# Kernel optimization log

Measured on AMD Instinct MI355X. Metric: run time of the kernel, lower is better.

## Reference

```python
import jax, jax.numpy as jnp
import numpy as np

HEAD_NUM = 8
EMB = 256
HEAD_SIZE = EMB // HEAD_NUM
POS_LEN = 128
ROPE_BASE = 100.0
LN_EPS = 1e-5
SOFTPICK_EPS = 1e-6


def _rope_tables():
    inv_freq = 1.0 / ROPE_BASE ** (jnp.arange(0, HEAD_SIZE, 2, dtype=jnp.float32) / HEAD_SIZE)
    t = jnp.arange(POS_LEN, dtype=jnp.float32)
    freqs = jnp.einsum('i,j->ij', t, inv_freq)          # [W, hs/2]
    freqs = jnp.concatenate([freqs, freqs], axis=-1)     # [W, hs]
    return jnp.sin(freqs), jnp.cos(freqs)


def _apply_rope(e, sin, cos):
    # e: [..., W, hs]; sin/cos: [W, hs]
    h = HEAD_SIZE // 2
    rot = jnp.concatenate([-e[..., h:], e[..., :h]], axis=-1)
    return e * cos + rot * sin


def _layernorm(x, g, b):
    mu = jnp.mean(x, axis=-1, keepdims=True)
    var = jnp.mean(jnp.square(x - mu), axis=-1, keepdims=True)
    return (x - mu) * jax.lax.rsqrt(var + LN_EPS) * g + b


def _softpick(x):
    m = jnp.max(x, axis=-1, keepdims=True)
    e = jnp.exp(x - m) - jnp.exp(-m)
    return jax.nn.relu(e) / (jnp.sum(jnp.abs(e), axis=-1, keepdims=True) + SOFTPICK_EPS)


def setup_inputs() -> dict:
    key = jax.random.key(0)
    ks = jax.random.split(key, 12)
    B, C, H, W = 4, EMB, 256, 128
    hn, hs = HEAD_NUM, HEAD_SIZE
    s = 0.02
    return {
        'left': jax.random.normal(ks[0], (B, C, H, W), jnp.float32),
        'right': jax.random.normal(ks[1], (B, C, H, W), jnp.float32),
        'qw': jax.random.normal(ks[2], (hn, hs, hs), jnp.float32) * s,   # grouped 1x1 conv weights
        'kw': jax.random.normal(ks[3], (hn, hs, hs), jnp.float32) * s,
        'vw': jax.random.normal(ks[4], (hn, hs, hs), jnp.float32) * s,
        'proj_w': jax.random.normal(ks[5], (C, C), jnp.float32) * s,
        'proj_b': jnp.zeros((C,), jnp.float32),
        'ln1_g': jnp.ones((C,), jnp.float32),
        'ln1_b': jnp.zeros((C,), jnp.float32),
        'ln2_g': jnp.ones((C,), jnp.float32),
        'ln2_b': jnp.zeros((C,), jnp.float32),
        'w1': jax.random.normal(ks[6], (C, 4 * C), jnp.float32) * s,
        'b1': jnp.zeros((4 * C,), jnp.float32),
        'w2': jax.random.normal(ks[7], (4 * C, C), jnp.float32) * s,
        'b2': jnp.zeros((C,), jnp.float32),
    }


def reference(left, right, qw, kw, vw, proj_w, proj_b,
              ln1_g, ln1_b, ln2_g, ln2_b, w1, b1, w2, b2):
    B, C, H, W = left.shape
    hn, hs = HEAD_NUM, HEAD_SIZE
    scale = hs ** -0.5
    sin, cos = _rope_tables()  # [W, hs]

    def grouped_proj(x, w):
        # grouped 1x1 conv -> per-head matmul; out [B, H, hn, W, hs]
        xr = x.reshape(B, hn, hs, H, W)
        return jnp.einsum('bgihw,goi->bhgwo', xr, w)

    q = _apply_rope(grouped_proj(left, qw), sin, cos)
    k = _apply_rope(grouped_proj(right, kw), sin, cos)
    v = grouped_proj(right, vw)

    att = _softpick(jnp.einsum('bhgqd,bhgkd->bhgqk', q, k) * scale)  # [B,H,hn,W,W]
    out = jnp.einsum('bhgqk,bhgkd->bhqgd', att, v).reshape(B, H, W, C)

    x1 = _layernorm(out @ proj_w + proj_b + jnp.transpose(left, (0, 2, 3, 1)), ln1_g, ln1_b)
    ffn = jax.nn.gelu(x1 @ w1 + b1, approximate=False) @ w2 + b2
    return _layernorm(ffn + x1, ln2_g, ln2_b)
```

## Files before the change

kernel.cpp:

```cpp
#include <hip/hip_runtime.h>
#include <hip/hip_bf16.h>

#define DEV __device__ __forceinline__

typedef __attribute__((ext_vector_type(8))) short bf16x8_t;
typedef __attribute__((ext_vector_type(4))) float f32x4_t;

constexpr int cB = 4, cC = 256, cH = 256, cW = 128, cHN = 8, cHS = 32;
constexpr int cM = cB * cH * cW;

DEV float bfu(unsigned int b16) { union { unsigned int u; float f; } v; v.u = b16 << 16; return v.f; }
DEV unsigned short f2bb(float f) { union { __hip_bfloat16 h; unsigned short u; } v; v.h = __float2bfloat16(f); return v.u; }
DEV unsigned int pk2(float a, float b) { return (unsigned)f2bb(a) | ((unsigned)f2bb(b) << 16); }

#define GLOAD_LDS16(g, l) \
  __builtin_amdgcn_global_load_lds((const __attribute__((address_space(1))) void*)(g), \
                                   (__attribute__((address_space(3))) void*)(l), 16, 0, 0)

DEV float gelu_fast(float v) {
  float ax = fabsf(v) * 0.7071067811865475f;
  float t = __builtin_amdgcn_rcpf(1.0f + 0.3275911f * ax);
  float poly = ((((1.061405429f * t - 1.453152027f) * t + 1.421413741f) * t
                 - 0.284496736f) * t + 0.254829592f) * t;
  float e = __expf(-ax * ax);
  float erfv = 1.0f - poly * e;
  float phi = 0.5f + 0.5f * copysignf(erfv, v);
  return v * phi;
}

__global__ __launch_bounds__(256) void transpose_bf16(const float* __restrict__ src,
                                                      __hip_bfloat16* __restrict__ dst,
                                                      int R, int Ccol) {
  int idx = blockIdx.x * 256 + threadIdx.x;
  if (idx < R * Ccol) {
    int r = idx / Ccol, c = idx - r * Ccol;
    dst[c * R + r] = __float2bfloat16(src[idx]);
  }
}

__global__ __launch_bounds__(256) void transpose_perm_bf16(const float* __restrict__ src,
                                                           __hip_bfloat16* __restrict__ dst,
                                                           int R, int Ccol) {
  int idx = blockIdx.x * 256 + threadIdx.x;
  if (idx < R * Ccol) {
    int r = idx / Ccol, c = idx - r * Ccol;
    int pk = (r & ~63) | ((r & 15) << 2) | ((r >> 4) & 3);
    dst[c * R + pk] = __float2bfloat16(src[idx]);
  }
}

__global__ __launch_bounds__(256) void rope_init(float2* __restrict__ tab) {
  int i = blockIdx.x * 256 + threadIdx.x;
  int w = i >> 4, c = i & 15;
  float inv = expf((float)c * -0.28782313662425572f);
  float ang = (float)w * inv;
  tab[i] = make_float2(sinf(ang), cosf(ang));
}

constexpr int XL_OFF = 0, XR_OFF = 10240, WQ_OFF = 20480, WK_OFF = 23040, WV_OFF = 25600;
constexpr int QS_OFF = 28160, KS_OFF = 38400, VT_OFF = 0, P_OFF = 10240;
constexpr int SMEM_BYTES = 48640;

__global__ __launch_bounds__(256) void attn_mfma(
    const float* __restrict__ left, const float* __restrict__ right,
    const float* __restrict__ qw, const float* __restrict__ kw, const float* __restrict__ vw,
    const float2* __restrict__ rope,
    __hip_bfloat16* __restrict__ att_out)
{
  __shared__ __align__(16) char smem[SMEM_BYTES];

  const int t = threadIdx.x;
  const int g = blockIdx.x & 7;
  const int h = (blockIdx.x >> 3) & 255;
  const int b = blockIdx.x >> 11;
  const size_t HW = (size_t)cH * cW;

  {
    const float* lb = left  + ((size_t)(b * cC + g * cHS) * cH + h) * cW;
    const float* rb = right + ((size_t)(b * cC + g * cHS) * cH + h) * cW;
    int w = t & 127, ih = (t >> 7) * 16;
    unsigned short* xlrow = (unsigned short*)(smem + XL_OFF) + w * 40 + ih;
    unsigned short* xrrow = (unsigned short*)(smem + XR_OFF) + w * 40 + ih;
#pragma unroll
    for (int i = 0; i < 16; i += 2) {
      float a0 = lb[(size_t)(ih + i) * HW + w], a1 = lb[(size_t)(ih + i + 1) * HW + w];
      *(unsigned int*)(xlrow + i) = pk2(a0, a1);
      float c0 = rb[(size_t)(ih + i) * HW + w], c1 = rb[(size_t)(ih + i + 1) * HW + w];
      *(unsigned int*)(xrrow + i) = pk2(c0, c1);
    }
    int o = t >> 3, i0 = (t & 7) * 4;
    {
      float4 v4 = *(const float4*)(qw + g * 1024 + t * 4);
      unsigned short* dst = (unsigned short*)(smem + WQ_OFF) + o * 40 + i0;
      *(unsigned int*)(dst) = pk2(v4.x, v4.y); *(unsigned int*)(dst + 2) = pk2(v4.z, v4.w);
    }
    {
      float4 v4 = *(const float4*)(kw + g * 1024 + t * 4);
      unsigned short* dst = (unsigned short*)(smem + WK_OFF) + o * 40 + i0;
      *(unsigned int*)(dst) = pk2(v4.x, v4.y); *(unsigned int*)(dst + 2) = pk2(v4.z, v4.w);
    }
    {
      float4 v4 = *(const float4*)(vw + g * 1024 + t * 4);
      unsigned short* dst = (unsigned short*)(smem + WV_OFF) + o * 40 + i0;
      *(unsigned int*)(dst) = pk2(v4.x, v4.y); *(unsigned int*)(dst + 2) = pk2(v4.z, v4.w);
    }
  }
  __syncthreads();

  const int lane = t & 63, wid = t >> 6;
  const int c = lane & 15, q4 = lane >> 4;
  const int wbase = wid * 32;
  const f32x4_t zero = {0.f, 0.f, 0.f, 0.f};

  bf16x8_t a_xl[2], a_xr[2];
#pragma unroll
  for (int sub = 0; sub < 2; ++sub) {
    a_xl[sub] = *(const bf16x8_t*)(smem + XL_OFF + (wbase + sub * 16 + c) * 80 + q4 * 16);
    a_xr[sub] = *(const bf16x8_t*)(smem + XR_OFF + (wbase + sub * 16 + c) * 80 + q4 * 16);
  }
  f32x4_t qacc[2][2], kacc[2][2];
#pragma unroll
  for (int ot = 0; ot < 2; ++ot) {
    bf16x8_t bq = *(const bf16x8_t*)(smem + WQ_OFF + (ot * 16 + c) * 80 + q4 * 16);
    bf16x8_t bk = *(const bf16x8_t*)(smem + WK_OFF + (ot * 16 + c) * 80 + q4 * 16);
#pragma unroll
    for (int sub = 0; sub < 2; ++sub) {
      qacc[sub][ot] = __builtin_amdgcn_mfma_f32_16x16x32_bf16(a_xl[sub], bq, zero, 0, 0, 0);
      kacc[sub][ot] = __builtin_amdgcn_mfma_f32_16x16x32_bf16(a_xr[sub], bk, zero, 0, 0, 0);
    }
  }
  {
    const float scale = 0.17677669529663687f;
    unsigned short* qsp = (unsigned short*)(smem + QS_OFF);
    unsigned short* ksp = (unsigned short*)(smem + KS_OFF);
#pragma unroll
    for (int sub = 0; sub < 2; ++sub)
#pragma unroll
      for (int r = 0; r < 4; ++r) {
        int w = wbase + sub * 16 + q4 * 4 + r;
        float2 sc = rope[w * 16 + c];
        float sn = sc.x, cs = sc.y;
        float q0 = qacc[sub][0][r], q1 = qacc[sub][1][r];
        qsp[w * 40 + c]      = f2bb((q0 * cs - q1 * sn) * scale);
        qsp[w * 40 + c + 16] = f2bb((q1 * cs + q0 * sn) * scale);
        float k0 = kacc[sub][0][r], k1 = kacc[sub][1][r];
        ksp[w * 40 + c]      = f2bb(k0 * cs - k1 * sn);
        ksp[w * 40 + c + 16] = f2bb(k1 * cs + k0 * sn);
      }
  }
  __syncthreads();

  {
    f32x4_t vacc[2][2];
#pragma unroll
    for (int dt = 0; dt < 2; ++dt) {
      bf16x8_t awv = *(const bf16x8_t*)(smem + WV_OFF + (dt * 16 + c) * 80 + q4 * 16);
#pragma unroll
      for (int sub = 0; sub < 2; ++sub)
        vacc[dt][sub] = __builtin_amdgcn_mfma_f32_16x16x32_bf16(awv, a_xr[sub], zero, 0, 0, 0);
    }
    unsigned short* vtp = (unsigned short*)(smem + VT_OFF);
#pragma unroll
    for (int dt = 0; dt < 2; ++dt)
#pragma unroll
      for (int r = 0; r < 4; ++r) {
        int d = dt * 16 + q4 * 4 + r;
        *(unsigned int*)(vtp + d * 136 + c * 8 + wid * 2) = pk2(vacc[dt][0][r], vacc[dt][1][r]);
      }
  }

  bf16x8_t aq0 = *(const bf16x8_t*)(smem + QS_OFF + (wbase + c) * 80 + q4 * 16);
  bf16x8_t aq1 = *(const bf16x8_t*)(smem + QS_OFF + (wbase + 16 + c) * 80 + q4 * 16);
  f32x4_t sac[2][8];
#pragma unroll
  for (int kt = 0; kt < 8; ++kt) {
    bf16x8_t bk = *(const bf16x8_t*)(smem + KS_OFF + (kt * 16 + c) * 80 + q4 * 16);
    sac[0][kt] = __builtin_amdgcn_mfma_f32_16x16x32_bf16(aq0, bk, zero, 0, 0, 0);
    sac[1][kt] = __builtin_amdgcn_mfma_f32_16x16x32_bf16(aq1, bk, zero, 0, 0, 0);
  }

  float dinv_[2][4];
#pragma unroll
  for (int sub = 0; sub < 2; ++sub)
#pragma unroll
    for (int r = 0; r < 4; ++r) {
      float m = sac[sub][0][r];
#pragma unroll
      for (int kt = 1; kt < 8; ++kt) m = fmaxf(m, sac[sub][kt][r]);
      m = fmaxf(m, __shfl_xor(m, 1));
      m = fmaxf(m, __shfl_xor(m, 2));
      m = fmaxf(m, __shfl_xor(m, 4));
      m = fmaxf(m, __shfl_xor(m, 8));
      float em = __expf(-m);
      float ss = 0.f;
#pragma unroll
      for (int kt = 0; kt < 8; ++kt) {
        float e = __expf(sac[sub][kt][r] - m) - em;
        sac[sub][kt][r] = fmaxf(e, 0.f);
        ss += fabsf(e);
      }
      ss += __shfl_xor(ss, 1);
      ss += __shfl_xor(ss, 2);
      ss += __shfl_xor(ss, 4);
      ss += __shfl_xor(ss, 8);
      dinv_[sub][r] = 1.0f / (ss + 1e-6f);
    }
  __syncthreads();

  {
    unsigned short* pp = (unsigned short*)(smem + P_OFF);
#pragma unroll
    for (int sub = 0; sub < 2; ++sub)
#pragma unroll
      for (int r = 0; r < 4; ++r) {
        int w = wbase + sub * 16 + q4 * 4 + r;
        float dv = dinv_[sub][r];
        uint4 u;
        u.x = pk2(sac[sub][0][r] * dv, sac[sub][1][r] * dv);
        u.y = pk2(sac[sub][2][r] * dv, sac[sub][3][r] * dv);
        u.z = pk2(sac[sub][4][r] * dv, sac[sub][5][r] * dv);
        u.w = pk2(sac[sub][6][r] * dv, sac[sub][7][r] * dv);
        *(uint4*)(pp + w * 136 + c * 8) = u;
      }
  }
  f32x4_t oacc[2][2] = {{zero, zero}, {zero, zero}};
#pragma unroll
  for (int ks = 0; ks < 4; ++ks) {
    bf16x8_t ap0 = *(const bf16x8_t*)(smem + P_OFF + (wbase + c) * 272 + ks * 64 + q4 * 16);
    bf16x8_t ap1 = *(const bf16x8_t*)(smem + P_OFF + (wbase + 16 + c) * 272 + ks * 64 + q4 * 16);
    bf16x8_t bv0 = *(const bf16x8_t*)(smem + VT_OFF + (c) * 272 + ks * 64 + q4 * 16);
    bf16x8_t bv1 = *(const bf16x8_t*)(smem + VT_OFF + (16 + c) * 272 + ks * 64 + q4 * 16);
    oacc[0][0] = __builtin_amdgcn_mfma_f32_16x16x32_bf16(ap0, bv0, oacc[0][0], 0, 0, 0);
    oacc[0][1] = __builtin_amdgcn_mfma_f32_16x16x32_bf16(ap0, bv1, oacc[0][1], 0, 0, 0);
    oacc[1][0] = __builtin_amdgcn_mfma_f32_16x16x32_bf16(ap1, bv0, oacc[1][0], 0, 0, 0);
    oacc[1][1] = __builtin_amdgcn_mfma_f32_16x16x32_bf16(ap1, bv1, oacc[1][1], 0, 0, 0);
  }
  {
    __hip_bfloat16* ob = att_out + ((size_t)(b * cH + h) * cW) * cC + g * cHS;
#pragma unroll
    for (int sub = 0; sub < 2; ++sub)
#pragma unroll
      for (int dt = 0; dt < 2; ++dt)
#pragma unroll
        for (int r = 0; r < 4; ++r) {
          int w = wbase + sub * 16 + q4 * 4 + r;
          ob[(size_t)w * cC + dt * 16 + c] = __float2bfloat16(oacc[sub][dt][r]);
        }
  }
}

__global__ __launch_bounds__(256) void ffn1_gemm(
    const __hip_bfloat16* __restrict__ A, const __hip_bfloat16* __restrict__ Bt,
    const float* __restrict__ bias, __hip_bfloat16* __restrict__ outb)
{
  constexpr int K = 256, N = 1024;
  __shared__ __align__(16) char smem[49152];
  const int t = threadIdx.x;
  const int id = blockIdx.x;
  const int slot = id >> 3;
  const int by = (id & 7) * 128 + (slot >> 3);
  const int bx = slot & 7;
  const int m0 = by * 128, n0 = bx * 128;
  const int lane = t & 63, wid = t >> 6;
  const int r16 = lane & 15, kq = lane >> 4;
  const int wr = (wid >> 1) * 64, wc = (wid & 1) * 64;

  f32x4_t acc[4][4];
#pragma unroll
  for (int fi = 0; fi < 4; ++fi)
#pragma unroll
    for (int fj = 0; fj < 4; ++fj) acc[fi][fj] = {0.f, 0.f, 0.f, 0.f};

  auto stage = [&](int buf, int k0) {
    char* As = smem + buf * 16384;
    char* Bs = As + 8192;
#pragma unroll
    for (int i = 0; i < 2; ++i) {
      int chunk = i * 4 + wid;
      int row = chunk * 16 + (lane >> 2);
      int sw = (((lane & 3) ^ ((row >> 1) & 3))) * 8;
      GLOAD_LDS16(A  + (size_t)(m0 + row) * K + k0 + sw, As + chunk * 1024);
      GLOAD_LDS16(Bt + (size_t)(n0 + row) * K + k0 + sw, Bs + chunk * 1024);
    }
  };

  constexpr int NK = K >> 5;
  stage(0, 0);
  stage(1, 32);
  for (int tt = 0; tt < NK; ++tt) {
    if (tt + 2 < NK) {
      stage((tt + 2) % 3, (tt + 2) << 5);
      asm volatile("s_waitcnt vmcnt(8)" ::: "memory");
    } else if (tt + 1 < NK) {
      asm volatile("s_waitcnt vmcnt(4)" ::: "memory");
    } else {
      asm volatile("s_waitcnt vmcnt(0)" ::: "memory");
    }
    __builtin_amdgcn_s_barrier();
    __builtin_amdgcn_sched_barrier(0);
    char* As = smem + (tt % 3) * 16384;
    char* Bs = As + 8192;
    bf16x8_t af[4], bf[4];
#pragma unroll
    for (int fi = 0; fi < 4; ++fi) {
      int rr = wr + fi * 16 + r16;
      af[fi] = *(const bf16x8_t*)(As + rr * 64 + ((kq ^ ((rr >> 1) & 3)) * 16));
    }
#pragma unroll
    for (int fj = 0; fj < 4; ++fj) {
      int rr = wc + fj * 16 + r16;
      bf[fj] = *(const bf16x8_t*)(Bs + rr * 64 + ((kq ^ ((rr >> 1) & 3)) * 16));
    }
#pragma unroll
    for (int fi = 0; fi < 4; ++fi)
#pragma unroll
      for (int fj = 0; fj < 4; ++fj)
        acc[fi][fj] = __builtin_amdgcn_mfma_f32_16x16x32_bf16(af[fi], bf[fj], acc[fi][fj], 0, 0, 0);
    __builtin_amdgcn_sched_barrier(0);
    __builtin_amdgcn_s_barrier();
  }

  float bv[4];
#pragma unroll
  for (int fj = 0; fj < 4; ++fj) bv[fj] = bias[n0 + wc + fj * 16 + r16];
  __hip_bfloat16* obase = outb + (size_t)(m0 + wr + kq * 4) * N + n0 + wc + r16 * 4;
#pragma unroll
  for (int fi = 0; fi < 4; ++fi)
#pragma unroll
    for (int r = 0; r < 4; ++r) {
      float v0 = gelu_fast(acc[fi][0][r] + bv[0]);
      float v1 = gelu_fast(acc[fi][1][r] + bv[1]);
      float v2 = gelu_fast(acc[fi][2][r] + bv[2]);
      float v3 = gelu_fast(acc[fi][3][r] + bv[3]);
      uint2 u;
      u.x = pk2(v0, v1);
      u.y = pk2(v2, v3);
      *(uint2*)(obase + (size_t)(fi * 16 + r) * N) = u;
    }
}

template<int KK, bool FFN2>
__global__ __launch_bounds__(256, 2) void gemm_ln(
    const __hip_bfloat16* __restrict__ A, const __hip_bfloat16* __restrict__ Bt,
    const float* __restrict__ bias, const float* __restrict__ leftres,
    const __hip_bfloat16* __restrict__ resbf,
    const float* __restrict__ g, const float* __restrict__ be,
    void* __restrict__ outp)
{
  __shared__ __align__(16) char smem[73728];
  const int t = threadIdx.x, lane = t & 63, wid = t >> 6;
  const int c = lane & 15, q4 = lane >> 4;
  const int m0 = blockIdx.x * 128;
  const int wr = wid * 32;
  const f32x4_t zero = {0.f, 0.f, 0.f, 0.f};

  f32x4_t acc[2][16];
#pragma unroll
  for (int fi = 0; fi < 2; ++fi)
#pragma unroll
    for (int fj = 0; fj < 16; ++fj) acc[fi][fj] = zero;

  auto stage = [&](int buf, int k0) {
    char* As = smem + buf * 24576;
    char* Bs = As + 8192;
#pragma unroll
    for (int i = 0; i < 2; ++i) {
      int chunk = (wid * 2 + i);
      int row = chunk * 16 + (lane >> 2);
      int sw = (((lane & 3) ^ ((row >> 1) & 3))) * 8;
      GLOAD_LDS16(A + (size_t)(m0 + row) * KK + k0 + sw, As + chunk * 1024);
    }
#pragma unroll
    for (int i = 0; i < 4; ++i) {
      int chunk = (wid * 4 + i);
      int row = chunk * 16 + (lane >> 2);
      int sw = (((lane & 3) ^ ((row >> 1) & 3))) * 8;
      GLOAD_LDS16(Bt + (size_t)row * KK + k0 + sw, Bs + chunk * 1024);
    }
  };

  constexpr int NK = KK >> 5;
  stage(0, 0);
  stage(1, 32);
  for (int tt = 0; tt < NK; ++tt) {
    if (tt + 2 < NK) {
      stage((tt + 2) % 3, (tt + 2) << 5);
      asm volatile("s_waitcnt vmcnt(12)" ::: "memory");
    } else if (tt + 1 < NK) {
      asm volatile("s_waitcnt vmcnt(6)" ::: "memory");
    } else {
      asm volatile("s_waitcnt vmcnt(0)" ::: "memory");
    }
    __builtin_amdgcn_s_barrier();
    __builtin_amdgcn_sched_barrier(0);
    char* As = smem + (tt % 3) * 24576;
    char* Bs = As + 8192;
    int ra0 = wr + c, ra1 = wr + 16 + c;
    bf16x8_t af0 = *(const bf16x8_t*)(As + ra0 * 64 + ((q4 ^ ((ra0 >> 1) & 3)) * 16));
    bf16x8_t af1 = *(const bf16x8_t*)(As + ra1 * 64 + ((q4 ^ ((ra1 >> 1) & 3)) * 16));
#pragma unroll
    for (int fj = 0; fj < 16; ++fj) {
      int rb = fj * 16 + c;
      bf16x8_t bf = *(const bf16x8_t*)(Bs + rb * 64 + ((q4 ^ ((rb >> 1) & 3)) * 16));
      acc[0][fj] = __builtin_amdgcn_mfma_f32_16x16x32_bf16(af0, bf, acc[0][fj], 0, 0, 0);
      acc[1][fj] = __builtin_amdgcn_mfma_f32_16x16x32_bf16(af1, bf, acc[1][fj], 0, 0, 0);
    }
    __builtin_amdgcn_sched_barrier(0);
    __builtin_amdgcn_s_barrier();
  }

  if (!FFN2) {
    const int b_ = m0 >> 15, h_ = (m0 >> 7) & 255;
#pragma unroll
    for (int fj = 0; fj < 16; ++fj) {
      int n = fj * 16 + c;
      float bv = bias[n];
#pragma unroll
      for (int fi = 0; fi < 2; ++fi) {
        int w0 = wr + fi * 16 + q4 * 4;
        float4 lr = *(const float4*)(leftres + (((size_t)b_ * 256 + n) * 256 + h_) * 128 + w0);
        float la[4] = {lr.x, lr.y, lr.z, lr.w};
#pragma unroll
        for (int r = 0; r < 4; ++r) acc[fi][fj][r] += bv + la[r];
      }
    }
  } else {
#pragma unroll
    for (int fj = 0; fj < 16; ++fj) {
      int n = fj * 16 + c;
      float bv = bias[n];
#pragma unroll
      for (int fi = 0; fi < 2; ++fi)
#pragma unroll
        for (int r = 0; r < 4; ++r) {
          int row = wr + fi * 16 + q4 * 4 + r;
          acc[fi][fj][r] += bv + __bfloat162float(resbf[(size_t)(m0 + row) * 256 + n]);
        }
    }
  }

  float mu[2][4], rs[2][4];
#pragma unroll
  for (int fi = 0; fi < 2; ++fi)
#pragma unroll
    for (int r = 0; r < 4; ++r) {
      float s = 0.f;
#pragma unroll
      for (int fj = 0; fj < 16; ++fj) s += acc[fi][fj][r];
      s += __shfl_xor(s, 1); s += __shfl_xor(s, 2); s += __shfl_xor(s, 4); s += __shfl_xor(s, 8);
      float m_ = s * (1.0f / 256.0f);
      float sq = 0.f;
#pragma unroll
      for (int fj = 0; fj < 16; ++fj) { float d = acc[fi][fj][r] - m_; sq += d * d; }
      sq += __shfl_xor(sq, 1); sq += __shfl_xor(sq, 2); sq += __shfl_xor(sq, 4); sq += __shfl_xor(sq, 8);
      mu[fi][r] = m_;
      rs[fi][r] = rsqrtf(sq * (1.0f / 256.0f) + 1e-5f);
    }
#pragma unroll
  for (int fj = 0; fj < 16; ++fj) {
    int n = fj * 16 + c;
    float gv = g[n], bev = be[n];
#pragma unroll
    for (int fi = 0; fi < 2; ++fi)
#pragma unroll
      for (int r = 0; r < 4; ++r) {
        int row = wr + fi * 16 + q4 * 4 + r;
        float val = (acc[fi][fj][r] - mu[fi][r]) * rs[fi][r] * gv + bev;
        if (FFN2)
          ((float*)outp)[(size_t)(m0 + row) * 256 + n] = val;
        else
          ((__hip_bfloat16*)outp)[(size_t)(m0 + row) * 256 + n] = __float2bfloat16(val);
      }
  }
}

extern "C" void kernel_launch(void* const* d_in, const int* in_sizes, int n_in,
                              void* d_out, int out_size, void* d_ws, size_t ws_size,
                              hipStream_t stream) {
  const float* left   = (const float*)d_in[0];
  const float* right  = (const float*)d_in[1];
  const float* qw     = (const float*)d_in[2];
  const float* kw     = (const float*)d_in[3];
  const float* vw     = (const float*)d_in[4];
  const float* proj_w = (const float*)d_in[5];
  const float* proj_b = (const float*)d_in[6];
  const float* ln1_g  = (const float*)d_in[7];
  const float* ln1_b  = (const float*)d_in[8];
  const float* ln2_g  = (const float*)d_in[9];
  const float* ln2_b  = (const float*)d_in[10];
  const float* w1     = (const float*)d_in[11];
  const float* b1     = (const float*)d_in[12];
  const float* w2     = (const float*)d_in[13];
  const float* b2     = (const float*)d_in[14];

  char* ws = (char*)d_ws;
  __hip_bfloat16* att_out = (__hip_bfloat16*)ws;
  __hip_bfloat16* x1      = (__hip_bfloat16*)(ws + 67108864);
  __hip_bfloat16* hidden  = (__hip_bfloat16*)(ws + 134217728);
  float2*         rope    = (float2*)(ws + 134217728);
  __hip_bfloat16* pwT     = (__hip_bfloat16*)(ws + 402653184);
  __hip_bfloat16* w1T     = pwT + 65536;
  __hip_bfloat16* w2T     = w1T + 262144;

  transpose_bf16<<<256, 256, 0, stream>>>(proj_w, pwT, 256, 256);
  transpose_bf16<<<1024, 256, 0, stream>>>(w1, w1T, 256, 1024);
  transpose_perm_bf16<<<1024, 256, 0, stream>>>(w2, w2T, 1024, 256);
  rope_init<<<8, 256, 0, stream>>>(rope);

  attn_mfma<<<cB * cH * cHN, 256, 0, stream>>>(left, right, qw, kw, vw, rope, att_out);

  gemm_ln<256, false><<<cM / 128, 256, 0, stream>>>(att_out, pwT, proj_b, left, nullptr,
                                                    ln1_g, ln1_b, x1);
  ffn1_gemm<<<8192, 256, 0, stream>>>(x1, w1T, b1, hidden);
  gemm_ln<1024, true><<<cM / 128, 256, 0, stream>>>(hidden, w2T, b2, nullptr, x1,
                                                    ln2_g, ln2_b, d_out);
}
```

Measured before the change: 445.1 us.

## Store FFN hidden and W2 in scaled FP8 and use FP8 MFMA for FFN2

The GELU output of FFN1 is now scaled by 64 and packed to FP8 instead of bf16, and W2 is transposed into scaled FP8. A new FFN2+LayerNorm kernel runs fp8×fp8 MFMA and unscales by 1/4096 before the residual and norm. This halves the dominant hidden-tensor traffic (written by FFN1, read by FFN2) and uses a higher-throughput MFMA path. The cost is lower precision, which risks accuracy against the reference tolerance.

```diff
diff --git a/kernel.cpp b/kernel.cpp
--- a/kernel.cpp
+++ b/kernel.cpp
@@ -38,14 +38,15 @@
   }
 }
 
-__global__ __launch_bounds__(256) void transpose_perm_bf16(const float* __restrict__ src,
-                                                           __hip_bfloat16* __restrict__ dst,
-                                                           int R, int Ccol) {
+__global__ __launch_bounds__(256) void transpose_perm_fp8(const float* __restrict__ src,
+                                                          unsigned char* __restrict__ dst,
+                                                          int R, int Ccol) {
   int idx = blockIdx.x * 256 + threadIdx.x;
   if (idx < R * Ccol) {
     int r = idx / Ccol, c = idx - r * Ccol;
     int pk = (r & ~63) | ((r & 15) << 2) | ((r >> 4) & 3);
-    dst[c * R + pk] = __float2bfloat16(src[idx]);
+    int u = __builtin_amdgcn_cvt_pk_fp8_f32(src[idx] * 64.0f, 0.0f, 0, false);
+    dst[(size_t)c * R + pk] = (unsigned char)(u & 0xff);
   }
 }
 
@@ -251,7 +252,7 @@
 
 __global__ __launch_bounds__(256) void ffn1_gemm(
     const __hip_bfloat16* __restrict__ A, const __hip_bfloat16* __restrict__ Bt,
-    const float* __restrict__ bias, __hip_bfloat16* __restrict__ outb)
+    const float* __restrict__ bias, unsigned char* __restrict__ outb)
 {
   constexpr int K = 256, N = 1024;
   __shared__ __align__(16) char smem[49152];
@@ -323,30 +324,28 @@
   float bv[4];
 #pragma unroll
   for (int fj = 0; fj < 4; ++fj) bv[fj] = bias[n0 + wc + fj * 16 + r16];
-  __hip_bfloat16* obase = outb + (size_t)(m0 + wr + kq * 4) * N + n0 + wc + r16 * 4;
+  unsigned char* obase = outb + (size_t)(m0 + wr + kq * 4) * N + n0 + wc + r16 * 4;
 #pragma unroll
   for (int fi = 0; fi < 4; ++fi)
 #pragma unroll
     for (int r = 0; r < 4; ++r) {
-      float v0 = gelu_fast(acc[fi][0][r] + bv[0]);
-      float v1 = gelu_fast(acc[fi][1][r] + bv[1]);
-      float v2 = gelu_fast(acc[fi][2][r] + bv[2]);
-      float v3 = gelu_fast(acc[fi][3][r] + bv[3]);
-      uint2 u;
-      u.x = pk2(v0, v1);
-      u.y = pk2(v2, v3);
-      *(uint2*)(obase + (size_t)(fi * 16 + r) * N) = u;
-    }
-}
-
-template<int KK, bool FFN2>
-__global__ __launch_bounds__(256, 2) void gemm_ln(
+      float v0 = gelu_fast(acc[fi][0][r] + bv[0]) * 64.0f;
+      float v1 = gelu_fast(acc[fi][1][r] + bv[1]) * 64.0f;
+      float v2 = gelu_fast(acc[fi][2][r] + bv[2]) * 64.0f;
+      float v3 = gelu_fast(acc[fi][3][r] + bv[3]) * 64.0f;
+      int u = __builtin_amdgcn_cvt_pk_fp8_f32(v0, v1, 0, false);
+      u = __builtin_amdgcn_cvt_pk_fp8_f32(v2, v3, u, true);
+      *(unsigned int*)(obase + (size_t)(fi * 16 + r) * N) = (unsigned)u;
+    }
+}
+
+__global__ __launch_bounds__(256, 2) void proj_gemm_ln(
     const __hip_bfloat16* __restrict__ A, const __hip_bfloat16* __restrict__ Bt,
     const float* __restrict__ bias, const float* __restrict__ leftres,
-    const __hip_bfloat16* __restrict__ resbf,
     const float* __restrict__ g, const float* __restrict__ be,
-    void* __restrict__ outp)
+    __hip_bfloat16* __restrict__ outp)
 {
+  constexpr int KK = 256;
   __shared__ __align__(16) char smem[73728];
   const int t = threadIdx.x, lane = t & 63, wid = t >> 6;
   const int c = lane & 15, q4 = lane >> 4;
@@ -409,7 +408,7 @@
     __builtin_amdgcn_s_barrier();
   }
 
-  if (!FFN2) {
+  {
     const int b_ = m0 >> 15, h_ = (m0 >> 7) & 255;
 #pragma unroll
     for (int fj = 0; fj < 16; ++fj) {
@@ -424,19 +423,6 @@
         for (int r = 0; r < 4; ++r) acc[fi][fj][r] += bv + la[r];
       }
     }
-  } else {
-#pragma unroll
-    for (int fj = 0; fj < 16; ++fj) {
-      int n = fj * 16 + c;
-      float bv = bias[n];
-#pragma unroll
-      for (int fi = 0; fi < 2; ++fi)
-#pragma unroll
-        for (int r = 0; r < 4; ++r) {
-          int row = wr + fi * 16 + q4 * 4 + r;
-          acc[fi][fj][r] += bv + __bfloat162float(resbf[(size_t)(m0 + row) * 256 + n]);
-        }
-    }
   }
 
   float mu[2][4], rs[2][4];
@@ -465,11 +451,132 @@
 #pragma unroll
       for (int r = 0; r < 4; ++r) {
         int row = wr + fi * 16 + q4 * 4 + r;
-        float val = (acc[fi][fj][r] - mu[fi][r]) * rs[fi][r] * gv + bev;
-        if (FFN2)
-          ((float*)outp)[(size_t)(m0 + row) * 256 + n] = val;
-        else
-          ((__hip_bfloat16*)outp)[(size_t)(m0 + row) * 256 + n] = __float2bfloat16(val);
+        outp[(size_t)(m0 + row) * 256 + n] =
+            __float2bfloat16((acc[fi][fj][r] - mu[fi][r]) * rs[fi][r] * gv + bev);
+      }
+  }
+}
+
+__global__ __launch_bounds__(256, 2) void ffn2_ln(
+    const unsigned char* __restrict__ A, const unsigned char* __restrict__ Bt,
+    const float* __restrict__ bias, const __hip_bfloat16* __restrict__ resbf,
+    const float* __restrict__ g, const float* __restrict__ be,
+    float* __restrict__ outp)
+{
+  constexpr int KK = 1024;
+  __shared__ __align__(16) char smem[73728];
+  const int t = threadIdx.x, lane = t & 63, wid = t >> 6;
+  const int c = lane & 15, q4 = lane >> 4;
+  const int m0 = blockIdx.x * 128;
+  const int wr = wid * 32;
+  const f32x4_t zero = {0.f, 0.f, 0.f, 0.f};
+
+  f32x4_t acc[2][16];
+#pragma unroll
+  for (int fi = 0; fi < 2; ++fi)
+#pragma unroll
+    for (int fj = 0; fj < 16; ++fj) acc[fi][fj] = zero;
+
+  auto stage = [&](int buf, int k0) {
+    char* As = smem + buf * 24576;
+    char* Bs = As + 8192;
+#pragma unroll
+    for (int i = 0; i < 2; ++i) {
+      int chunk = (wid * 2 + i);
+      int row = chunk * 16 + (lane >> 2);
+      int sw = (((lane & 3) ^ ((row >> 1) & 3))) * 16;
+      GLOAD_LDS16(A + (size_t)(m0 + row) * KK + k0 + sw, As + chunk * 1024);
+    }
+#pragma unroll
+    for (int i = 0; i < 4; ++i) {
+      int chunk = (wid * 4 + i);
+      int row = chunk * 16 + (lane >> 2);
+      int sw = (((lane & 3) ^ ((row >> 1) & 3))) * 16;
+      GLOAD_LDS16(Bt + (size_t)row * KK + k0 + sw, Bs + chunk * 1024);
+    }
+  };
+
+  constexpr int NK = 16;
+  stage(0, 0);
+  stage(1, 64);
+  const int sl = (c >> 1) & 3;
+  const int koff0 = ((((q4 >> 1)) ^ sl) << 4) | ((q4 & 1) << 3);
+  const int koff1 = (((2 | (q4 >> 1)) ^ sl) << 4) | ((q4 & 1) << 3);
+  for (int tt = 0; tt < NK; ++tt) {
+    if (tt + 2 < NK) {
+      stage((tt + 2) % 3, (tt + 2) << 6);
+      asm volatile("s_waitcnt vmcnt(12)" ::: "memory");
+    } else if (tt + 1 < NK) {
+      asm volatile("s_waitcnt vmcnt(6)" ::: "memory");
+    } else {
+      asm volatile("s_waitcnt vmcnt(0)" ::: "memory");
+    }
+    __builtin_amdgcn_s_barrier();
+    __builtin_amdgcn_sched_barrier(0);
+    char* As = smem + (tt % 3) * 24576;
+    char* Bs = As + 8192;
+    const char* arow0 = As + (wr + c) * 64;
+    const char* arow1 = As + (wr + 16 + c) * 64;
+    long a00 = *(const long*)(arow0 + koff0);
+    long a01 = *(const long*)(arow0 + koff1);
+    long a10 = *(const long*)(arow1 + koff0);
+    long a11 = *(const long*)(arow1 + koff1);
+#pragma unroll
+    for (int fj = 0; fj < 16; ++fj) {
+      const char* brow = Bs + (fj * 16 + c) * 64;
+      long b0 = *(const long*)(brow + koff0);
+      long b1 = *(const long*)(brow + koff1);
+      acc[0][fj] = __builtin_amdgcn_mfma_f32_16x16x32_fp8_fp8(a00, b0, acc[0][fj], 0, 0, 0);
+      acc[0][fj] = __builtin_amdgcn_mfma_f32_16x16x32_fp8_fp8(a01, b1, acc[0][fj], 0, 0, 0);
+      acc[1][fj] = __builtin_amdgcn_mfma_f32_16x16x32_fp8_fp8(a10, b0, acc[1][fj], 0, 0, 0);
+      acc[1][fj] = __builtin_amdgcn_mfma_f32_16x16x32_fp8_fp8(a11, b1, acc[1][fj], 0, 0, 0);
+    }
+    __builtin_amdgcn_sched_barrier(0);
+    __builtin_amdgcn_s_barrier();
+  }
+
+#pragma unroll
+  for (int fj = 0; fj < 16; ++fj) {
+    int n = fj * 16 + c;
+    float bv = bias[n];
+#pragma unroll
+    for (int fi = 0; fi < 2; ++fi)
+#pragma unroll
+      for (int r = 0; r < 4; ++r) {
+        int row = wr + fi * 16 + q4 * 4 + r;
+        acc[fi][fj][r] = acc[fi][fj][r] * 0.000244140625f + bv +
+                         __bfloat162float(resbf[(size_t)(m0 + row) * 256 + n]);
+      }
+  }
+
+  float mu[2][4], rs[2][4];
+#pragma unroll
+  for (int fi = 0; fi < 2; ++fi)
+#pragma unroll
+    for (int r = 0; r < 4; ++r) {
+      float s = 0.f;
+#pragma unroll
+      for (int fj = 0; fj < 16; ++fj) s += acc[fi][fj][r];
+      s += __shfl_xor(s, 1); s += __shfl_xor(s, 2); s += __shfl_xor(s, 4); s += __shfl_xor(s, 8);
+      float m_ = s * (1.0f / 256.0f);
+      float sq = 0.f;
+#pragma unroll
+      for (int fj = 0; fj < 16; ++fj) { float d = acc[fi][fj][r] - m_; sq += d * d; }
+      sq += __shfl_xor(sq, 1); sq += __shfl_xor(sq, 2); sq += __shfl_xor(sq, 4); sq += __shfl_xor(sq, 8);
+      mu[fi][r] = m_;
+      rs[fi][r] = rsqrtf(sq * (1.0f / 256.0f) + 1e-5f);
+    }
+#pragma unroll
+  for (int fj = 0; fj < 16; ++fj) {
+    int n = fj * 16 + c;
+    float gv = g[n], bev = be[n];
+#pragma unroll
+    for (int fi = 0; fi < 2; ++fi)
+#pragma unroll
+      for (int r = 0; r < 4; ++r) {
+        int row = wr + fi * 16 + q4 * 4 + r;
+        outp[(size_t)(m0 + row) * 256 + n] =
+            (acc[fi][fj][r] - mu[fi][r]) * rs[fi][r] * gv + bev;
       }
   }
 }
@@ -496,22 +603,20 @@
   char* ws = (char*)d_ws;
   __hip_bfloat16* att_out = (__hip_bfloat16*)ws;
   __hip_bfloat16* x1      = (__hip_bfloat16*)(ws + 67108864);
-  __hip_bfloat16* hidden  = (__hip_bfloat16*)(ws + 134217728);
+  unsigned char*  hidden  = (unsigned char*)(ws + 134217728);
   float2*         rope    = (float2*)(ws + 134217728);
   __hip_bfloat16* pwT     = (__hip_bfloat16*)(ws + 402653184);
   __hip_bfloat16* w1T     = pwT + 65536;
-  __hip_bfloat16* w2T     = w1T + 262144;
+  unsigned char*  w2T     = (unsigned char*)(w1T + 262144);
 
   transpose_bf16<<<256, 256, 0, stream>>>(proj_w, pwT, 256, 256);
   transpose_bf16<<<1024, 256, 0, stream>>>(w1, w1T, 256, 1024);
-  transpose_perm_bf16<<<1024, 256, 0, stream>>>(w2, w2T, 1024, 256);
+  transpose_perm_fp8<<<1024, 256, 0, stream>>>(w2, w2T, 1024, 256);
   rope_init<<<8, 256, 0, stream>>>(rope);
 
   attn_mfma<<<cB * cH * cHN, 256, 0, stream>>>(left, right, qw, kw, vw, rope, att_out);
 
-  gemm_ln<256, false><<<cM / 128, 256, 0, stream>>>(att_out, pwT, proj_b, left, nullptr,
-                                                    ln1_g, ln1_b, x1);
+  proj_gemm_ln<<<cM / 128, 256, 0, stream>>>(att_out, pwT, proj_b, left, ln1_g, ln1_b, x1);
   ffn1_gemm<<<8192, 256, 0, stream>>>(x1, w1T, b1, hidden);
-  gemm_ln<1024, true><<<cM / 128, 256, 0, stream>>>(hidden, w2T, b2, nullptr, x1,
-                                                    ln2_g, ln2_b, d_out);
-}
+  ffn2_ln<<<cM / 128, 256, 0, stream>>>(hidden, w2T, b2, x1, ln2_g, ln2_b, (float*)d_out);
+}
```

Measured after the change: 406.4 us, median of 2. -8.7%, faster.

## Fuse FFN1 GEMM+GELU with FFN2 GEMM+LayerNorm into one kernel

Applied to the files above, without the earlier changes.

The separate FFN1 GEMM (which wrote a 1024-wide bf16 hidden tensor to global memory) and the FFN2 GEMM+LN kernel are replaced by a single kernel. Each block keeps a 128-row x1 tile in LDS and loops over 32-column hidden chunks, computing GELU(x1·W1) into LDS and accumulating it straight into the 256-wide output accumulators. The residual is read from the LDS copy of x1, and the w2 permutation changes to suit the 32-wide k-chunks. This removes the large hidden-tensor round trip through HBM, but uses about 136KB of LDS, so only one block fits per CU, and adds barriers inside every chunk iteration.

```diff
diff --git a/kernel.cpp b/kernel.cpp
--- a/kernel.cpp
+++ b/kernel.cpp
@@ -38,14 +38,14 @@
   }
 }
 
-__global__ __launch_bounds__(256) void transpose_perm_bf16(const float* __restrict__ src,
-                                                           __hip_bfloat16* __restrict__ dst,
-                                                           int R, int Ccol) {
+__global__ __launch_bounds__(256) void transpose_perm32_bf16(const float* __restrict__ src,
+                                                             __hip_bfloat16* __restrict__ dst,
+                                                             int R, int Ccol) {
   int idx = blockIdx.x * 256 + threadIdx.x;
   if (idx < R * Ccol) {
     int r = idx / Ccol, c = idx - r * Ccol;
-    int pk = (r & ~63) | ((r & 15) << 2) | ((r >> 4) & 3);
-    dst[c * R + pk] = __float2bfloat16(src[idx]);
+    int pk = (r & ~31) | ((r & 15) << 1) | ((r >> 4) & 1);
+    dst[(size_t)c * R + pk] = __float2bfloat16(src[idx]);
   }
 }
 
@@ -249,104 +249,13 @@
   }
 }
 
-__global__ __launch_bounds__(256) void ffn1_gemm(
-    const __hip_bfloat16* __restrict__ A, const __hip_bfloat16* __restrict__ Bt,
-    const float* __restrict__ bias, __hip_bfloat16* __restrict__ outb)
-{
-  constexpr int K = 256, N = 1024;
-  __shared__ __align__(16) char smem[49152];
-  const int t = threadIdx.x;
-  const int id = blockIdx.x;
-  const int slot = id >> 3;
-  const int by = (id & 7) * 128 + (slot >> 3);
-  const int bx = slot & 7;
-  const int m0 = by * 128, n0 = bx * 128;
-  const int lane = t & 63, wid = t >> 6;
-  const int r16 = lane & 15, kq = lane >> 4;
-  const int wr = (wid >> 1) * 64, wc = (wid & 1) * 64;
-
-  f32x4_t acc[4][4];
-#pragma unroll
-  for (int fi = 0; fi < 4; ++fi)
-#pragma unroll
-    for (int fj = 0; fj < 4; ++fj) acc[fi][fj] = {0.f, 0.f, 0.f, 0.f};
-
-  auto stage = [&](int buf, int k0) {
-    char* As = smem + buf * 16384;
-    char* Bs = As + 8192;
-#pragma unroll
-    for (int i = 0; i < 2; ++i) {
-      int chunk = i * 4 + wid;
-      int row = chunk * 16 + (lane >> 2);
-      int sw = (((lane & 3) ^ ((row >> 1) & 3))) * 8;
-      GLOAD_LDS16(A  + (size_t)(m0 + row) * K + k0 + sw, As + chunk * 1024);
-      GLOAD_LDS16(Bt + (size_t)(n0 + row) * K + k0 + sw, Bs + chunk * 1024);
-    }
-  };
-
-  constexpr int NK = K >> 5;
-  stage(0, 0);
-  stage(1, 32);
-  for (int tt = 0; tt < NK; ++tt) {
-    if (tt + 2 < NK) {
-      stage((tt + 2) % 3, (tt + 2) << 5);
-      asm volatile("s_waitcnt vmcnt(8)" ::: "memory");
-    } else if (tt + 1 < NK) {
-      asm volatile("s_waitcnt vmcnt(4)" ::: "memory");
-    } else {
-      asm volatile("s_waitcnt vmcnt(0)" ::: "memory");
-    }
-    __builtin_amdgcn_s_barrier();
-    __builtin_amdgcn_sched_barrier(0);
-    char* As = smem + (tt % 3) * 16384;
-    char* Bs = As + 8192;
-    bf16x8_t af[4], bf[4];
-#pragma unroll
-    for (int fi = 0; fi < 4; ++fi) {
-      int rr = wr + fi * 16 + r16;
-      af[fi] = *(const bf16x8_t*)(As + rr * 64 + ((kq ^ ((rr >> 1) & 3)) * 16));
-    }
-#pragma unroll
-    for (int fj = 0; fj < 4; ++fj) {
-      int rr = wc + fj * 16 + r16;
-      bf[fj] = *(const bf16x8_t*)(Bs + rr * 64 + ((kq ^ ((rr >> 1) & 3)) * 16));
-    }
-#pragma unroll
-    for (int fi = 0; fi < 4; ++fi)
-#pragma unroll
-      for (int fj = 0; fj < 4; ++fj)
-        acc[fi][fj] = __builtin_amdgcn_mfma_f32_16x16x32_bf16(af[fi], bf[fj], acc[fi][fj], 0, 0, 0);
-    __builtin_amdgcn_sched_barrier(0);
-    __builtin_amdgcn_s_barrier();
-  }
-
-  float bv[4];
-#pragma unroll
-  for (int fj = 0; fj < 4; ++fj) bv[fj] = bias[n0 + wc + fj * 16 + r16];
-  __hip_bfloat16* obase = outb + (size_t)(m0 + wr + kq * 4) * N + n0 + wc + r16 * 4;
-#pragma unroll
-  for (int fi = 0; fi < 4; ++fi)
-#pragma unroll
-    for (int r = 0; r < 4; ++r) {
-      float v0 = gelu_fast(acc[fi][0][r] + bv[0]);
-      float v1 = gelu_fast(acc[fi][1][r] + bv[1]);
-      float v2 = gelu_fast(acc[fi][2][r] + bv[2]);
-      float v3 = gelu_fast(acc[fi][3][r] + bv[3]);
-      uint2 u;
-      u.x = pk2(v0, v1);
-      u.y = pk2(v2, v3);
-      *(uint2*)(obase + (size_t)(fi * 16 + r) * N) = u;
-    }
-}
-
-template<int KK, bool FFN2>
-__global__ __launch_bounds__(256, 2) void gemm_ln(
+__global__ __launch_bounds__(256, 2) void proj_gemm_ln(
     const __hip_bfloat16* __restrict__ A, const __hip_bfloat16* __restrict__ Bt,
     const float* __restrict__ bias, const float* __restrict__ leftres,
-    const __hip_bfloat16* __restrict__ resbf,
     const float* __restrict__ g, const float* __restrict__ be,
-    void* __restrict__ outp)
+    __hip_bfloat16* __restrict__ outp)
 {
+  constexpr int KK = 256;
   __shared__ __align__(16) char smem[73728];
   const int t = threadIdx.x, lane = t & 63, wid = t >> 6;
   const int c = lane & 15, q4 = lane >> 4;
@@ -409,7 +318,7 @@
     __builtin_amdgcn_s_barrier();
   }
 
-  if (!FFN2) {
+  {
     const int b_ = m0 >> 15, h_ = (m0 >> 7) & 255;
 #pragma unroll
     for (int fj = 0; fj < 16; ++fj) {
@@ -424,19 +333,6 @@
         for (int r = 0; r < 4; ++r) acc[fi][fj][r] += bv + la[r];
       }
     }
-  } else {
-#pragma unroll
-    for (int fj = 0; fj < 16; ++fj) {
-      int n = fj * 16 + c;
-      float bv = bias[n];
-#pragma unroll
-      for (int fi = 0; fi < 2; ++fi)
-#pragma unroll
-        for (int r = 0; r < 4; ++r) {
-          int row = wr + fi * 16 + q4 * 4 + r;
-          acc[fi][fj][r] += bv + __bfloat162float(resbf[(size_t)(m0 + row) * 256 + n]);
-        }
-    }
   }
 
   float mu[2][4], rs[2][4];
@@ -465,11 +361,164 @@
 #pragma unroll
       for (int r = 0; r < 4; ++r) {
         int row = wr + fi * 16 + q4 * 4 + r;
-        float val = (acc[fi][fj][r] - mu[fi][r]) * rs[fi][r] * gv + bev;
-        if (FFN2)
-          ((float*)outp)[(size_t)(m0 + row) * 256 + n] = val;
-        else
-          ((__hip_bfloat16*)outp)[(size_t)(m0 + row) * 256 + n] = __float2bfloat16(val);
+        outp[(size_t)(m0 + row) * 256 + n] =
+            __float2bfloat16((acc[fi][fj][r] - mu[fi][r]) * rs[fi][r] * gv + bev);
+      }
+  }
+}
+
+__global__ __launch_bounds__(256, 1) void ffn_fused2(
+    const __hip_bfloat16* __restrict__ x1g, const __hip_bfloat16* __restrict__ w1T,
+    const __hip_bfloat16* __restrict__ w2T, const float* __restrict__ b1,
+    const float* __restrict__ b2, const float* __restrict__ g2, const float* __restrict__ be2,
+    float* __restrict__ outp)
+{
+  __shared__ __align__(16) char smem[139264];
+  char* X1  = smem;
+  char* W1b = smem + 65536;
+  char* W2b = smem + 98304;
+  char* H   = smem + 131072;
+
+  const int t = threadIdx.x, lane = t & 63, wid = t >> 6;
+  const int c = lane & 15, q4 = lane >> 4;
+  const int m0 = blockIdx.x * 128;
+  const int wr = wid * 32;
+  const f32x4_t zero = {0.f, 0.f, 0.f, 0.f};
+  const int sw8 = c & 7;
+  const int sw4 = (c >> 1) & 3;
+
+#pragma unroll
+  for (int i = 0; i < 16; ++i) {
+    int L = i * 256 + t;
+    int row = L >> 5, s = lane & 31;
+    int gsl = s ^ (row & 7);
+    GLOAD_LDS16(x1g + (size_t)(m0 + row) * 256 + gsl * 8, X1 + (i * 4096 + wid * 1024));
+  }
+
+  auto stageW = [&](int buf, int j) {
+    char* W1 = W1b + buf * 16384;
+    char* W2 = W2b + buf * 16384;
+#pragma unroll
+    for (int i = 0; i < 4; ++i) {
+      int L = i * 256 + t;
+      int row = L >> 5, s = lane & 31;
+      int gsl = s ^ (row & 7);
+      GLOAD_LDS16(w1T + (size_t)(j * 32 + row) * 256 + gsl * 8, W1 + (i * 4096 + wid * 1024));
+    }
+#pragma unroll
+    for (int i = 0; i < 4; ++i) {
+      int L = i * 256 + t;
+      int row = L >> 2, s = lane & 3;
+      int gsl = s ^ ((row >> 1) & 3);
+      GLOAD_LDS16(w2T + (size_t)row * 1024 + j * 32 + gsl * 8, W2 + (i * 4096 + wid * 1024));
+    }
+  };
+  stageW(0, 0);
+
+  f32x4_t acc[2][16];
+#pragma unroll
+  for (int fi = 0; fi < 2; ++fi)
+#pragma unroll
+    for (int fj = 0; fj < 16; ++fj) acc[fi][fj] = zero;
+
+  for (int j = 0; j < 32; ++j) {
+    if (j + 1 < 32) {
+      stageW((j + 1) & 1, j + 1);
+      asm volatile("s_waitcnt vmcnt(8)" ::: "memory");
+    } else {
+      asm volatile("s_waitcnt vmcnt(0)" ::: "memory");
+    }
+    __builtin_amdgcn_s_barrier();
+    __builtin_amdgcn_sched_barrier(0);
+
+    char* W1 = W1b + (j & 1) * 16384;
+    f32x4_t hacc[2][2] = {{zero, zero}, {zero, zero}};
+#pragma unroll
+    for (int kk = 0; kk < 8; ++kk) {
+      int sl = (kk * 4 + q4) ^ sw8;
+      bf16x8_t a0 = *(const bf16x8_t*)(X1 + (wr + c) * 512 + sl * 16);
+      bf16x8_t a1 = *(const bf16x8_t*)(X1 + (wr + 16 + c) * 512 + sl * 16);
+      bf16x8_t b0 = *(const bf16x8_t*)(W1 + (c) * 512 + sl * 16);
+      bf16x8_t b1f = *(const bf16x8_t*)(W1 + (16 + c) * 512 + sl * 16);
+      hacc[0][0] = __builtin_amdgcn_mfma_f32_16x16x32_bf16(a0, b0, hacc[0][0], 0, 0, 0);
+      hacc[0][1] = __builtin_amdgcn_mfma_f32_16x16x32_bf16(a0, b1f, hacc[0][1], 0, 0, 0);
+      hacc[1][0] = __builtin_amdgcn_mfma_f32_16x16x32_bf16(a1, b0, hacc[1][0], 0, 0, 0);
+      hacc[1][1] = __builtin_amdgcn_mfma_f32_16x16x32_bf16(a1, b1f, hacc[1][1], 0, 0, 0);
+    }
+
+    float b1v0 = b1[j * 32 + c], b1v1 = b1[j * 32 + 16 + c];
+#pragma unroll
+    for (int fi = 0; fi < 2; ++fi)
+#pragma unroll
+      for (int r = 0; r < 4; ++r) {
+        int row = wr + fi * 16 + q4 * 4 + r;
+        float v0 = gelu_fast(hacc[fi][0][r] + b1v0);
+        float v1 = gelu_fast(hacc[fi][1][r] + b1v1);
+        int swv = (q4 * 2 + (r >> 1)) & 3;
+        *(unsigned int*)(H + row * 64 + (((c >> 2) ^ swv) * 16) + (c & 3) * 4) = pk2(v0, v1);
+      }
+    __builtin_amdgcn_sched_barrier(0);
+    asm volatile("s_waitcnt lgkmcnt(0)" ::: "memory");
+    __builtin_amdgcn_s_barrier();
+    __builtin_amdgcn_sched_barrier(0);
+
+    char* W2 = W2b + (j & 1) * 16384;
+    int slh = q4 ^ sw4;
+    bf16x8_t ha0 = *(const bf16x8_t*)(H + (wr + c) * 64 + slh * 16);
+    bf16x8_t ha1 = *(const bf16x8_t*)(H + (wr + 16 + c) * 64 + slh * 16);
+#pragma unroll
+    for (int fj = 0; fj < 16; ++fj) {
+      int rb = fj * 16 + c;
+      bf16x8_t wb = *(const bf16x8_t*)(W2 + rb * 64 + ((q4 ^ ((rb >> 1) & 3)) * 16));
+      acc[0][fj] = __builtin_amdgcn_mfma_f32_16x16x32_bf16(ha0, wb, acc[0][fj], 0, 0, 0);
+      acc[1][fj] = __builtin_amdgcn_mfma_f32_16x16x32_bf16(ha1, wb, acc[1][fj], 0, 0, 0);
+    }
+    __builtin_amdgcn_sched_barrier(0);
+  }
+
+#pragma unroll
+  for (int fj = 0; fj < 16; ++fj) {
+    int n = fj * 16 + c;
+    float bv = b2[n];
+#pragma unroll
+    for (int fi = 0; fi < 2; ++fi)
+#pragma unroll
+      for (int r = 0; r < 4; ++r) {
+        int row = wr + fi * 16 + q4 * 4 + r;
+        int swr = (q4 * 4 + r) & 7;
+        int gsl = (fj * 2 + (c >> 3)) ^ swr;
+        unsigned short rv = *(unsigned short*)(X1 + row * 512 + gsl * 16 + (c & 7) * 2);
+        acc[fi][fj][r] += bv + bfu(rv);
+      }
+  }
+  float mu[2][4], rs[2][4];
+#pragma unroll
+  for (int fi = 0; fi < 2; ++fi)
+#pragma unroll
+    for (int r = 0; r < 4; ++r) {
+      float s = 0.f;
+#pragma unroll
+      for (int fj = 0; fj < 16; ++fj) s += acc[fi][fj][r];
+      s += __shfl_xor(s, 1); s += __shfl_xor(s, 2); s += __shfl_xor(s, 4); s += __shfl_xor(s, 8);
+      float m_ = s * (1.0f / 256.0f);
+      float sq = 0.f;
+#pragma unroll
+      for (int fj = 0; fj < 16; ++fj) { float d = acc[fi][fj][r] - m_; sq += d * d; }
+      sq += __shfl_xor(sq, 1); sq += __shfl_xor(sq, 2); sq += __shfl_xor(sq, 4); sq += __shfl_xor(sq, 8);
+      mu[fi][r] = m_;
+      rs[fi][r] = rsqrtf(sq * (1.0f / 256.0f) + 1e-5f);
+    }
+#pragma unroll
+  for (int fj = 0; fj < 16; ++fj) {
+    int n = fj * 16 + c;
+    float gv = g2[n], bev = be2[n];
+#pragma unroll
+    for (int fi = 0; fi < 2; ++fi)
+#pragma unroll
+      for (int r = 0; r < 4; ++r) {
+        int row = wr + fi * 16 + q4 * 4 + r;
+        outp[(size_t)(m0 + row) * 256 + n] =
+            (acc[fi][fj][r] - mu[fi][r]) * rs[fi][r] * gv + bev;
       }
   }
 }
@@ -496,7 +545,6 @@
   char* ws = (char*)d_ws;
   __hip_bfloat16* att_out = (__hip_bfloat16*)ws;
   __hip_bfloat16* x1      = (__hip_bfloat16*)(ws + 67108864);
-  __hip_bfloat16* hidden  = (__hip_bfloat16*)(ws + 134217728);
   float2*         rope    = (float2*)(ws + 134217728);
   __hip_bfloat16* pwT     = (__hip_bfloat16*)(ws + 402653184);
   __hip_bfloat16* w1T     = pwT + 65536;
@@ -504,14 +552,11 @@
 
   transpose_bf16<<<256, 256, 0, stream>>>(proj_w, pwT, 256, 256);
   transpose_bf16<<<1024, 256, 0, stream>>>(w1, w1T, 256, 1024);
-  transpose_perm_bf16<<<1024, 256, 0, stream>>>(w2, w2T, 1024, 256);
+  transpose_perm32_bf16<<<1024, 256, 0, stream>>>(w2, w2T, 1024, 256);
   rope_init<<<8, 256, 0, stream>>>(rope);
 
   attn_mfma<<<cB * cH * cHN, 256, 0, stream>>>(left, right, qw, kw, vw, rope, att_out);
 
-  gemm_ln<256, false><<<cM / 128, 256, 0, stream>>>(att_out, pwT, proj_b, left, nullptr,
-                                                    ln1_g, ln1_b, x1);
-  ffn1_gemm<<<8192, 256, 0, stream>>>(x1, w1T, b1, hidden);
-  gemm_ln<1024, true><<<cM / 128, 256, 0, stream>>>(hidden, w2T, b2, nullptr, x1,
-                                                    ln2_g, ln2_b, d_out);
-}
+  proj_gemm_ln<<<cM / 128, 256, 0, stream>>>(att_out, pwT, proj_b, left, ln1_g, ln1_b, x1);
+  ffn_fused2<<<cM / 128, 256, 0, stream>>>(x1, w1T, w2T, b1, b2, ln2_g, ln2_b, (float*)d_out);
+}
```

New measurement: 478.0 us. 7.4% more time.
